# Kernel tuning notes

Measured on AMD Instinct MI355X. Metric: run time of the kernel, lower is better.

The kernel has to match this reference:

```python
import jax, jax.numpy as jnp
import numpy as np

N = 50000
E = 800000
F_IN = 128
HID = 64
G = 512
NEG_SLOPE = 0.2


def setup_inputs() -> dict:
    key = jax.random.key(0)
    ks = jax.random.split(key, 24)
    g = lambda i, shape: jax.random.normal(ks[i], shape, dtype=jnp.float32) * 0.1
    inp = {
        "x": jax.random.normal(ks[0], (N, F_IN), dtype=jnp.float32),
        "edge_index": jax.random.randint(ks[1], (2, E), 0, N),
        "edge_weight": jax.random.uniform(ks[2], (E, 1), dtype=jnp.float32),
        "batch": jnp.sort(jax.random.randint(ks[3], (N,), 0, G)),
        # layer 1
        "W1": g(4, (F_IN, HID)), "as1": g(5, (HID,)), "ad1": g(6, (HID,)),
        "We1": g(7, (1, HID)), "ae1": g(8, (HID,)), "b1": jnp.zeros((HID,), jnp.float32),
        # layer 2
        "W2": g(9, (HID, HID)), "as2": g(10, (HID,)), "ad2": g(11, (HID,)),
        "We2": g(12, (1, HID)), "ae2": g(13, (HID,)), "b2": jnp.zeros((HID,), jnp.float32),
        # layer 3
        "W3": g(14, (HID, HID)), "as3": g(15, (HID,)), "ad3": g(16, (HID,)),
        "We3": g(17, (1, HID)), "ae3": g(18, (HID,)), "b3": jnp.zeros((HID,), jnp.float32),
        # readout
        "lin_w": g(19, (HID, 1)), "lin_b": jnp.zeros((1,), jnp.float32),
    }
    return inp


def gat_layer(x, src, dst, eattr, W, att_s, att_d, We, att_e, bias):
    # x: [N,Fin]; src/dst: [Et]; eattr: [Et,1]
    h = x @ W                                  # [N,HID]
    a_src = h @ att_s                          # [N]
    a_dst = h @ att_d                          # [N]
    a_edge = (eattr @ We) @ att_e              # [Et]
    alpha = a_src[src] + a_dst[dst] + a_edge   # [Et]
    alpha = jax.nn.leaky_relu(alpha, NEG_SLOPE)
    # segment softmax over incoming edges of each dst node
    m = jax.ops.segment_max(alpha, dst, num_segments=N)
    alpha = jnp.exp(alpha - m[dst])
    s = jax.ops.segment_sum(alpha, dst, num_segments=N)
    alpha = alpha / (s[dst] + 1e-16)
    # weighted scatter-add of source features
    out = jax.ops.segment_sum(h[src] * alpha[:, None], dst, num_segments=N)
    return out + bias


def reference(x, edge_index, edge_weight, batch,
              W1, as1, ad1, We1, ae1, b1,
              W2, as2, ad2, We2, ae2, b2,
              W3, as3, ad3, We3, ae3, b3,
              lin_w, lin_b):
    # PyG GATConv default: add self-loops with edge_attr fill_value='mean'
    loop = jnp.arange(N)
    src = jnp.concatenate([edge_index[0], loop])
    dst = jnp.concatenate([edge_index[1], loop])
    mean_attr = jnp.mean(edge_weight, axis=0, keepdims=True)  # [1,1]
    eattr = jnp.concatenate([edge_weight, jnp.broadcast_to(mean_attr, (N, 1))], axis=0)

    h = gat_layer(x, src, dst, eattr, W1, as1, ad1, We1, ae1, b1)
    h = jax.nn.relu(h)
    h = gat_layer(h, src, dst, eattr, W2, as2, ad2, We2, ae2, b2)
    h = jax.nn.relu(h)
    h = gat_layer(h, src, dst, eattr, W3, as3, ad3, We3, ae3, b3)

    # global mean pool over graphs
    sums = jax.ops.segment_sum(h, batch, num_segments=G)          # [G,HID]
    counts = jax.ops.segment_sum(jnp.ones((N,), h.dtype), batch, num_segments=G)
    pooled = sums / jnp.maximum(counts, 1.0)[:, None]
    # dropout p=0.6 is identity at inference
    out = pooled @ lin_w + lin_b                                   # [G,1]
    return jax.nn.sigmoid(out)
```

## Files before the change

kernel.cpp:

```cpp
#include <hip/hip_runtime.h>
#include <math.h>

#define N_NODES 50000
#define N_EDGES 800000
#define F_IN_DIM 128
#define HID 64
#define NG 512
#define NEG 0.2f
#define SLICE ((N_NODES + 7) / 8)
#define EPB 2048
#define CAP 64

static __device__ __forceinline__ float wave_sum(float v) {
    for (int o = 32; o; o >>= 1) v += __shfl_xor(v, o, 64);
    return v;
}

static __device__ __forceinline__ unsigned short f2bf(float f) {
    union { float f; unsigned u; } v; v.f = f;
    unsigned r = (v.u + 0x7FFF + ((v.u >> 16) & 1)) >> 16;
    return (unsigned short)r;
}
static __device__ __forceinline__ float bf2f(unsigned short b) {
    union { unsigned u; float f; } v; v.u = ((unsigned)b) << 16;
    return v.f;
}

__global__ __launch_bounds__(256) void scatter_all_k(
        const int* __restrict__ ei, const float* __restrict__ ew,
        int* __restrict__ deg, unsigned* __restrict__ bucket,
        uint2* __restrict__ ovf, int* __restrict__ ovf_cnt,
        float* __restrict__ mean_acc,
        const float* __restrict__ We1, const float* __restrict__ ae1,
        const float* __restrict__ We2, const float* __restrict__ ae2,
        const float* __restrict__ We3, const float* __restrict__ ae3,
        float* __restrict__ ce) {
    int grp = blockIdx.x >> 3, slice = blockIdx.x & 7;
    int lo = slice * SLICE, hi = lo + SLICE;
    int base = grp * EPB;
    int lim = min(base + EPB, N_EDGES);
    float s = 0.f;
    for (int e = base + threadIdx.x; e < lim; e += 256) {
        int dst = ei[N_EDGES + e];
        if (slice == 0) s += ew[e];
        if (dst >= lo && dst < hi) {
            int src = ei[e];
            float w = ew[e];
            int pos = atomicAdd(&deg[dst], 1);
            unsigned entry = (unsigned)(src & 0xFFFF) | ((unsigned)f2bf(w) << 16);
            if (pos < CAP) bucket[(dst << 6) + pos] = entry;
            else { int op = atomicAdd(ovf_cnt, 1); ovf[op] = make_uint2((unsigned)dst, entry); }
        }
    }
    int lane = threadIdx.x & 63, wv = threadIdx.x >> 6;
    if (slice == 0) {
        s = wave_sum(s);
        __shared__ float tmp[4];
        if (lane == 0) tmp[wv] = s;
        __syncthreads();
        if (threadIdx.x == 0) atomicAdd(mean_acc, tmp[0] + tmp[1] + tmp[2] + tmp[3]);
    }
    if (blockIdx.x == 0 && wv >= 1) {
        const float* We = (wv == 1) ? We1 : (wv == 2) ? We2 : We3;
        const float* ae = (wv == 1) ? ae1 : (wv == 2) ? ae2 : ae3;
        float v = We[lane] * ae[lane];
        v = wave_sum(v);
        if (lane == 0) ce[wv - 1] = v;
    }
}

__global__ __launch_bounds__(256) void gemm_att_k(
        const float* __restrict__ X, int F,
        const float* __restrict__ W,
        const float* __restrict__ as_, const float* __restrict__ ad_,
        unsigned short* __restrict__ H, float* __restrict__ Asrc,
        float* __restrict__ Adst) {
    extern __shared__ float smem[];
    float* Ws = smem;
    float* Xs = smem + F * HID;
    const int tid = threadIdx.x;
    const int tx = tid & 15, ty = tid >> 4;
    const int rowBase = blockIdx.x * 64;

    {
        const float4* W4 = (const float4*)W;
        float4* Ws4 = (float4*)Ws;
        int n4 = (F * HID) >> 2;
        for (int i = tid; i < n4; i += 256) Ws4[i] = W4[i];
    }

    float4 acc0 = {0,0,0,0}, acc1 = {0,0,0,0}, acc2 = {0,0,0,0}, acc3 = {0,0,0,0};

    const int xrow = tid >> 2;
    const int xkq  = tid & 3;
    const int nkt = F >> 4;

    for (int kt = 0; kt < nkt; ++kt) {
        __syncthreads();
        int k0 = kt << 4;
        int grow = rowBase + xrow;
        float4 xv = {0,0,0,0};
        if (grow < N_NODES)
            xv = *(const float4*)(X + (size_t)grow * F + k0 + (xkq << 2));
        float* xd = Xs + xrow * 17 + (xkq << 2);
        xd[0] = xv.x; xd[1] = xv.y; xd[2] = xv.z; xd[3] = xv.w;
        __syncthreads();

        #pragma unroll
        for (int kk = 0; kk < 16; ++kk) {
            float4 b = *(const float4*)&Ws[(k0 + kk) * HID + (tx << 2)];
            float a0 = Xs[(ty * 4 + 0) * 17 + kk];
            float a1 = Xs[(ty * 4 + 1) * 17 + kk];
            float a2 = Xs[(ty * 4 + 2) * 17 + kk];
            float a3 = Xs[(ty * 4 + 3) * 17 + kk];
            acc0.x += a0 * b.x; acc0.y += a0 * b.y; acc0.z += a0 * b.z; acc0.w += a0 * b.w;
            acc1.x += a1 * b.x; acc1.y += a1 * b.y; acc1.z += a1 * b.z; acc1.w += a1 * b.w;
            acc2.x += a2 * b.x; acc2.y += a2 * b.y; acc2.z += a2 * b.z; acc2.w += a2 * b.w;
            acc3.x += a3 * b.x; acc3.y += a3 * b.y; acc3.z += a3 * b.z; acc3.w += a3 * b.w;
        }
    }

    float4 as4 = *(const float4*)(as_ + (tx << 2));
    float4 ad4 = *(const float4*)(ad_ + (tx << 2));
    float4 accs[4] = {acc0, acc1, acc2, acc3};
    #pragma unroll
    for (int i = 0; i < 4; ++i) {
        int row = rowBase + ty * 4 + i;
        if (row >= N_NODES) break;
        float4 a = accs[i];
        ushort4 hv;
        hv.x = f2bf(a.x); hv.y = f2bf(a.y); hv.z = f2bf(a.z); hv.w = f2bf(a.w);
        *(ushort4*)(H + (size_t)row * HID + (tx << 2)) = hv;
        float vs = a.x * as4.x + a.y * as4.y + a.z * as4.z + a.w * as4.w;
        float vd = a.x * ad4.x + a.y * ad4.y + a.z * ad4.z + a.w * ad4.w;
        #pragma unroll
        for (int o = 8; o; o >>= 1) { vs += __shfl_xor(vs, o, 64); vd += __shfl_xor(vd, o, 64); }
        if (tx == 0) { Asrc[row] = vs; Adst[row] = vd; }
    }
}

__global__ __launch_bounds__(256) void aggregate_k(
        const unsigned short* __restrict__ H, const int* __restrict__ degArr,
        const unsigned* __restrict__ bucket,
        const uint2* __restrict__ ovf, const int* __restrict__ ovf_cnt_p,
        const float* __restrict__ Asrc, const float* __restrict__ Adst,
        const float* __restrict__ ceArr, int ci,
        const float* __restrict__ mean_acc,
        const float* __restrict__ bias, float* __restrict__ Out,
        int do_relu) {
    __shared__ float lp[16][64];
    __shared__ int   ls[16][64];
    int wv = threadIdx.x >> 6, lane = threadIdx.x & 63;
    int qid = lane >> 4, qlane = lane & 15;
    int slot = wv * 4 + qid;
    int n = blockIdx.x * 16 + slot;
    if (n >= N_NODES) return;
    int deg = degArr[n];
    int start = n << 6;
    float c = ceArr[ci];
    float ad = Adst[n];
    float mv = mean_acc[0] * (1.0f / (float)N_EDGES);
    float4 acc = {0, 0, 0, 0};
    float denom;

    float a_self = Asrc[n] + ad + c * mv;
    a_self = (a_self > 0.f) ? a_self : NEG * a_self;
    float p_self = __expf(a_self);

    if (deg <= CAP) {
        float lsum = 0.f;
        #pragma unroll
        for (int t = 0; t < 4; ++t) {
            int j = qlane + (t << 4);
            float p = 0.f; int s = 0;
            if (j < deg) {
                unsigned e = bucket[start + j];
                s = e & 0xFFFF;
                float a = Asrc[s] + ad + c * bf2f((unsigned short)(e >> 16));
                a = (a > 0.f) ? a : NEG * a;
                p = __expf(a);
                lsum += p;
            }
            lp[slot][j] = p;
            ls[slot][j] = s;
        }
        if (qlane == 0) lsum += p_self;
        #pragma unroll
        for (int o = 1; o < 16; o <<= 1) lsum += __shfl_xor(lsum, o, 64);
        denom = lsum;
        __builtin_amdgcn_wave_barrier();
        int dpad = (deg + 7) & ~7;
        for (int j = 0; j < dpad; j += 8) {
            float4 p0 = *(float4*)&lp[slot][j];
            float4 p1 = *(float4*)&lp[slot][j + 4];
            int4 s0 = *(int4*)&ls[slot][j];
            int4 s1 = *(int4*)&ls[slot][j + 4];
            ushort4 r0 = *(const ushort4*)(H + (size_t)s0.x * HID + (qlane << 2));
            ushort4 r1 = *(const ushort4*)(H + (size_t)s0.y * HID + (qlane << 2));
            ushort4 r2 = *(const ushort4*)(H + (size_t)s0.z * HID + (qlane << 2));
            ushort4 r3 = *(const ushort4*)(H + (size_t)s0.w * HID + (qlane << 2));
            ushort4 r4 = *(const ushort4*)(H + (size_t)s1.x * HID + (qlane << 2));
            ushort4 r5 = *(const ushort4*)(H + (size_t)s1.y * HID + (qlane << 2));
            ushort4 r6 = *(const ushort4*)(H + (size_t)s1.z * HID + (qlane << 2));
            ushort4 r7 = *(const ushort4*)(H + (size_t)s1.w * HID + (qlane << 2));
            acc.x += p0.x*bf2f(r0.x) + p0.y*bf2f(r1.x) + p0.z*bf2f(r2.x) + p0.w*bf2f(r3.x)
                   + p1.x*bf2f(r4.x) + p1.y*bf2f(r5.x) + p1.z*bf2f(r6.x) + p1.w*bf2f(r7.x);
            acc.y += p0.x*bf2f(r0.y) + p0.y*bf2f(r1.y) + p0.z*bf2f(r2.y) + p0.w*bf2f(r3.y)
                   + p1.x*bf2f(r4.y) + p1.y*bf2f(r5.y) + p1.z*bf2f(r6.y) + p1.w*bf2f(r7.y);
            acc.z += p0.x*bf2f(r0.z) + p0.y*bf2f(r1.z) + p0.z*bf2f(r2.z) + p0.w*bf2f(r3.z)
                   + p1.x*bf2f(r4.z) + p1.y*bf2f(r5.z) + p1.z*bf2f(r6.z) + p1.w*bf2f(r7.z);
            acc.w += p0.x*bf2f(r0.w) + p0.y*bf2f(r1.w) + p0.z*bf2f(r2.w) + p0.w*bf2f(r3.w)
                   + p1.x*bf2f(r4.w) + p1.y*bf2f(r5.w) + p1.z*bf2f(r6.w) + p1.w*bf2f(r7.w);
        }
    } else {
        int novf = *ovf_cnt_p;
        float lsum = 0.f;
        #pragma unroll
        for (int t = 0; t < 4; ++t) {
            int j = qlane + (t << 4);
            unsigned e = bucket[start + j];
            int s = e & 0xFFFF;
            float a = Asrc[s] + ad + c * bf2f((unsigned short)(e >> 16));
            a = (a > 0.f) ? a : NEG * a;
            float p = __expf(a);
            lsum += p;
            lp[slot][j] = p;
            ls[slot][j] = s;
        }
        __builtin_amdgcn_wave_barrier();
        for (int j = 0; j < 64; j += 8) {
            float4 p0 = *(float4*)&lp[slot][j];
            float4 p1 = *(float4*)&lp[slot][j + 4];
            int4 s0 = *(int4*)&ls[slot][j];
            int4 s1 = *(int4*)&ls[slot][j + 4];
            ushort4 r0 = *(const ushort4*)(H + (size_t)s0.x * HID + (qlane << 2));
            ushort4 r1 = *(const ushort4*)(H + (size_t)s0.y * HID + (qlane << 2));
            ushort4 r2 = *(const ushort4*)(H + (size_t)s0.z * HID + (qlane << 2));
            ushort4 r3 = *(const ushort4*)(H + (size_t)s0.w * HID + (qlane << 2));
            ushort4 r4 = *(const ushort4*)(H + (size_t)s1.x * HID + (qlane << 2));
            ushort4 r5 = *(const ushort4*)(H + (size_t)s1.y * HID + (qlane << 2));
            ushort4 r6 = *(const ushort4*)(H + (size_t)s1.z * HID + (qlane << 2));
            ushort4 r7 = *(const ushort4*)(H + (size_t)s1.w * HID + (qlane << 2));
            acc.x += p0.x*bf2f(r0.x) + p0.y*bf2f(r1.x) + p0.z*bf2f(r2.x) + p0.w*bf2f(r3.x)
                   + p1.x*bf2f(r4.x) + p1.y*bf2f(r5.x) + p1.z*bf2f(r6.x) + p1.w*bf2f(r7.x);
            acc.y += p0.x*bf2f(r0.y) + p0.y*bf2f(r1.y) + p0.z*bf2f(r2.y) + p0.w*bf2f(r3.y)
                   + p1.x*bf2f(r4.y) + p1.y*bf2f(r5.y) + p1.z*bf2f(r6.y) + p1.w*bf2f(r7.y);
            acc.z += p0.x*bf2f(r0.z) + p0.y*bf2f(r1.z) + p0.z*bf2f(r2.z) + p0.w*bf2f(r3.z)
                   + p1.x*bf2f(r4.z) + p1.y*bf2f(r5.z) + p1.z*bf2f(r6.z) + p1.w*bf2f(r7.z);
            acc.w += p0.x*bf2f(r0.w) + p0.y*bf2f(r1.w) + p0.z*bf2f(r2.w) + p0.w*bf2f(r3.w)
                   + p1.x*bf2f(r4.w) + p1.y*bf2f(r5.w) + p1.z*bf2f(r6.w) + p1.w*bf2f(r7.w);
        }
        for (int i = 0; i < novf; ++i) {
            uint2 o = ovf[i];
            if ((int)o.x == n) {
                unsigned e = o.y;
                int s = e & 0xFFFF;
                float a = Asrc[s] + ad + c * bf2f((unsigned short)(e >> 16));
                a = (a > 0.f) ? a : NEG * a;
                float p = __expf(a);
                if (qlane == 0) lsum += p;
                ushort4 r = *(const ushort4*)(H + (size_t)s * HID + (qlane << 2));
                acc.x += p * bf2f(r.x); acc.y += p * bf2f(r.y);
                acc.z += p * bf2f(r.z); acc.w += p * bf2f(r.w);
            }
        }
        if (qlane == 0) lsum += p_self;
        #pragma unroll
        for (int o = 1; o < 16; o <<= 1) lsum += __shfl_xor(lsum, o, 64);
        denom = lsum;
    }

    {
        ushort4 r = *(const ushort4*)(H + (size_t)n * HID + (qlane << 2));
        acc.x += p_self * bf2f(r.x); acc.y += p_self * bf2f(r.y);
        acc.z += p_self * bf2f(r.z); acc.w += p_self * bf2f(r.w);
    }

    float inv = 1.f / (denom + 1e-16f);
    float4 b4 = *(const float4*)(bias + (qlane << 2));
    acc.x = acc.x * inv + b4.x;
    acc.y = acc.y * inv + b4.y;
    acc.z = acc.z * inv + b4.z;
    acc.w = acc.w * inv + b4.w;
    if (do_relu) {
        acc.x = fmaxf(acc.x, 0.f); acc.y = fmaxf(acc.y, 0.f);
        acc.z = fmaxf(acc.z, 0.f); acc.w = fmaxf(acc.w, 0.f);
    }
    *(float4*)(Out + (size_t)n * HID + (qlane << 2)) = acc;
}

__global__ __launch_bounds__(256) void pool_readout_k(
        const float* __restrict__ act, const int* __restrict__ batch,
        const float* __restrict__ lin_w, const float* __restrict__ lin_b,
        float* __restrict__ out) {
    int wv = threadIdx.x >> 6, lane = threadIdx.x & 63;
    int g = blockIdx.x * 4 + wv;
    if (g >= NG) return;
    int lo = 0, hi = N_NODES;
    while (lo < hi) { int m = (lo + hi) >> 1; if (batch[m] < g) lo = m + 1; else hi = m; }
    int start = lo;
    hi = N_NODES;
    while (lo < hi) { int m = (lo + hi) >> 1; if (batch[m] < g + 1) lo = m + 1; else hi = m; }
    int end = lo;
    float acc = 0.f;
    int n = start;
    for (; n + 4 <= end; n += 4) {
        float v0 = act[(size_t)n * HID + lane];
        float v1 = act[(size_t)(n + 1) * HID + lane];
        float v2 = act[(size_t)(n + 2) * HID + lane];
        float v3 = act[(size_t)(n + 3) * HID + lane];
        acc += v0 + v1 + v2 + v3;
    }
    for (; n < end; ++n) acc += act[(size_t)n * HID + lane];
    float cntf = (float)(end - start);
    float v = acc / fmaxf(cntf, 1.f) * lin_w[lane];
    v = wave_sum(v);
    if (lane == 0) {
        float z = v + lin_b[0];
        out[g] = 1.f / (1.f + __expf(-z));
    }
}

extern "C" void kernel_launch(void* const* d_in, const int* in_sizes, int n_in,
                              void* d_out, int out_size, void* d_ws, size_t ws_size,
                              hipStream_t stream) {
    const float* x     = (const float*)d_in[0];
    const int*   ei    = (const int*)d_in[1];
    const float* ew    = (const float*)d_in[2];
    const int*   batch = (const int*)d_in[3];
    const float* W1  = (const float*)d_in[4];
    const float* as1 = (const float*)d_in[5];
    const float* ad1 = (const float*)d_in[6];
    const float* We1 = (const float*)d_in[7];
    const float* ae1 = (const float*)d_in[8];
    const float* b1  = (const float*)d_in[9];
    const float* W2  = (const float*)d_in[10];
    const float* as2 = (const float*)d_in[11];
    const float* ad2 = (const float*)d_in[12];
    const float* We2 = (const float*)d_in[13];
    const float* ae2 = (const float*)d_in[14];
    const float* b2  = (const float*)d_in[15];
    const float* W3  = (const float*)d_in[16];
    const float* as3 = (const float*)d_in[17];
    const float* ad3 = (const float*)d_in[18];
    const float* We3 = (const float*)d_in[19];
    const float* ae3 = (const float*)d_in[20];
    const float* b3  = (const float*)d_in[21];
    const float* lin_w = (const float*)d_in[22];
    const float* lin_b = (const float*)d_in[23];
    float* out = (float*)d_out;

    char* w = (char*)d_ws;
    size_t off = 0;
    auto alloc = [&](size_t bytes) -> void* {
        void* p = w + off;
        off = (off + bytes + 255) & ~(size_t)255;
        return p;
    };
    int*   deg      = (int*)alloc(N_NODES * sizeof(int));
    float* mean_acc = (float*)alloc(sizeof(float));
    int*   ovf_cnt  = (int*)alloc(sizeof(int));
    size_t zero_bytes = off;
    float* ce      = (float*)alloc(4 * sizeof(float));
    unsigned* bucket = (unsigned*)alloc((size_t)N_NODES * CAP * sizeof(unsigned));
    uint2* ovf     = (uint2*)alloc((size_t)N_EDGES * sizeof(uint2));
    float* a_src   = (float*)alloc(N_NODES * sizeof(float));
    float* a_dst   = (float*)alloc(N_NODES * sizeof(float));
    unsigned short* hbuf = (unsigned short*)alloc((size_t)N_NODES * HID * sizeof(unsigned short));
    float* actA    = (float*)alloc((size_t)N_NODES * HID * sizeof(float));
    float* actB    = (float*)alloc((size_t)N_NODES * HID * sizeof(float));

    hipMemsetAsync(d_ws, 0, zero_bytes, stream);

    int xgrid = ((N_EDGES + EPB - 1) / EPB) * 8;
    scatter_all_k<<<xgrid, 256, 0, stream>>>(ei, ew, deg, bucket, ovf, ovf_cnt,
                                             mean_acc, We1, ae1, We2, ae2, We3, ae3, ce);

    int ggrid = (N_NODES + 63) / 64;
    int agrid = (N_NODES + 15) / 16;

    size_t lds1 = (size_t)(F_IN_DIM * HID + 64 * 17) * sizeof(float);
    size_t lds2 = (size_t)(HID * HID + 64 * 17) * sizeof(float);

    gemm_att_k<<<ggrid, 256, lds1, stream>>>(x, F_IN_DIM, W1, as1, ad1, hbuf, a_src, a_dst);
    aggregate_k<<<agrid, 256, 0, stream>>>(hbuf, deg, bucket, ovf, ovf_cnt,
                                           a_src, a_dst, ce, 0, mean_acc, b1, actA, 1);
    gemm_att_k<<<ggrid, 256, lds2, stream>>>(actA, HID, W2, as2, ad2, hbuf, a_src, a_dst);
    aggregate_k<<<agrid, 256, 0, stream>>>(hbuf, deg, bucket, ovf, ovf_cnt,
                                           a_src, a_dst, ce, 1, mean_acc, b2, actB, 1);
    gemm_att_k<<<ggrid, 256, lds2, stream>>>(actB, HID, W3, as3, ad3, hbuf, a_src, a_dst);
    aggregate_k<<<agrid, 256, 0, stream>>>(hbuf, deg, bucket, ovf, ovf_cnt,
                                           a_src, a_dst, ce, 2, mean_acc, b3, actA, 0);

    pool_readout_k<<<NG / 4, 256, 0, stream>>>(actA, batch, lin_w, lin_b, out);
}
```

Baseline: 286.1 us.

## Merge edge scatter and layer-1 GEMM into one heterogeneous launch

The edge-bucketing scatter kernel and the first-layer feature GEMM now share a single launch. Blocks below XGRID do the scatter and the remaining blocks compute the GEMM, since neither depends on the other. The layer-1 GEMM also changes from staging all of W in LDS to streaming 16-row K-tiles of W alongside X tiles, which cuts LDS use. The aim is to remove one launch and let the atomic-heavy scatter overlap with the compute-bound GEMM; the cost is an extra branch and mixed block behaviour within one grid.

```diff
diff --git a/kernel.cpp b/kernel.cpp
--- a/kernel.cpp
+++ b/kernel.cpp
@@ -10,6 +10,8 @@
 #define SLICE ((N_NODES + 7) / 8)
 #define EPB 2048
 #define CAP 64
+#define XGRID (((N_EDGES + EPB - 1) / EPB) * 8)
+#define GGRID ((N_NODES + 63) / 64)
 
 static __device__ __forceinline__ float wave_sum(float v) {
     for (int o = 32; o; o >>= 1) v += __shfl_xor(v, o, 64);
@@ -26,7 +28,7 @@
     return v.f;
 }
 
-__global__ __launch_bounds__(256) void scatter_all_k(
+__global__ __launch_bounds__(256) void scatter_gemm1_k(
         const int* __restrict__ ei, const float* __restrict__ ew,
         int* __restrict__ deg, unsigned* __restrict__ bucket,
         uint2* __restrict__ ovf, int* __restrict__ ovf_cnt,
@@ -34,38 +36,104 @@
         const float* __restrict__ We1, const float* __restrict__ ae1,
         const float* __restrict__ We2, const float* __restrict__ ae2,
         const float* __restrict__ We3, const float* __restrict__ ae3,
-        float* __restrict__ ce) {
-    int grp = blockIdx.x >> 3, slice = blockIdx.x & 7;
-    int lo = slice * SLICE, hi = lo + SLICE;
-    int base = grp * EPB;
-    int lim = min(base + EPB, N_EDGES);
-    float s = 0.f;
-    for (int e = base + threadIdx.x; e < lim; e += 256) {
-        int dst = ei[N_EDGES + e];
-        if (slice == 0) s += ew[e];
-        if (dst >= lo && dst < hi) {
-            int src = ei[e];
-            float w = ew[e];
-            int pos = atomicAdd(&deg[dst], 1);
-            unsigned entry = (unsigned)(src & 0xFFFF) | ((unsigned)f2bf(w) << 16);
-            if (pos < CAP) bucket[(dst << 6) + pos] = entry;
-            else { int op = atomicAdd(ovf_cnt, 1); ovf[op] = make_uint2((unsigned)dst, entry); }
-        }
-    }
-    int lane = threadIdx.x & 63, wv = threadIdx.x >> 6;
-    if (slice == 0) {
-        s = wave_sum(s);
-        __shared__ float tmp[4];
-        if (lane == 0) tmp[wv] = s;
+        float* __restrict__ ce,
+        const float* __restrict__ X, const float* __restrict__ W,
+        const float* __restrict__ as_, const float* __restrict__ ad_,
+        unsigned short* __restrict__ H, float* __restrict__ Asrc,
+        float* __restrict__ Adst) {
+    extern __shared__ float smem[];
+    const int tid = threadIdx.x;
+
+    if (blockIdx.x < XGRID) {
+        int grp = blockIdx.x >> 3, slice = blockIdx.x & 7;
+        int lo = slice * SLICE, hi = lo + SLICE;
+        int base = grp * EPB;
+        int lim = min(base + EPB, N_EDGES);
+        float s = 0.f;
+        for (int e = base + tid; e < lim; e += 256) {
+            int dst = ei[N_EDGES + e];
+            if (slice == 0) s += ew[e];
+            if (dst >= lo && dst < hi) {
+                int src = ei[e];
+                float w = ew[e];
+                int pos = atomicAdd(&deg[dst], 1);
+                unsigned entry = (unsigned)(src & 0xFFFF) | ((unsigned)f2bf(w) << 16);
+                if (pos < CAP) bucket[(dst << 6) + pos] = entry;
+                else { int op = atomicAdd(ovf_cnt, 1); ovf[op] = make_uint2((unsigned)dst, entry); }
+            }
+        }
+        int lane = tid & 63, wv = tid >> 6;
+        if (slice == 0) {
+            s = wave_sum(s);
+            if (lane == 0) smem[wv] = s;
+            __syncthreads();
+            if (tid == 0) atomicAdd(mean_acc, smem[0] + smem[1] + smem[2] + smem[3]);
+        }
+        if (blockIdx.x == 0 && wv >= 1) {
+            const float* We = (wv == 1) ? We1 : (wv == 2) ? We2 : We3;
+            const float* ae = (wv == 1) ? ae1 : (wv == 2) ? ae2 : ae3;
+            float v = We[lane] * ae[lane];
+            v = wave_sum(v);
+            if (lane == 0) ce[wv - 1] = v;
+        }
+        return;
+    }
+
+    float* Xs = smem;
+    float* Wt = smem + 64 * 17;
+    const int tx = tid & 15, ty = tid >> 4;
+    const int bid = blockIdx.x - XGRID;
+    const int rowBase = bid * 64;
+
+    float4 acc0 = {0,0,0,0}, acc1 = {0,0,0,0}, acc2 = {0,0,0,0}, acc3 = {0,0,0,0};
+    const int xrow = tid >> 2;
+    const int xkq  = tid & 3;
+    const float4* W4 = (const float4*)W;
+    float4* Wt4 = (float4*)Wt;
+
+    #pragma unroll 2
+    for (int kt = 0; kt < (F_IN_DIM >> 4); ++kt) {
         __syncthreads();
-        if (threadIdx.x == 0) atomicAdd(mean_acc, tmp[0] + tmp[1] + tmp[2] + tmp[3]);
-    }
-    if (blockIdx.x == 0 && wv >= 1) {
-        const float* We = (wv == 1) ? We1 : (wv == 2) ? We2 : We3;
-        const float* ae = (wv == 1) ? ae1 : (wv == 2) ? ae2 : ae3;
-        float v = We[lane] * ae[lane];
-        v = wave_sum(v);
-        if (lane == 0) ce[wv - 1] = v;
+        int k0 = kt << 4;
+        int grow = rowBase + xrow;
+        float4 xv = {0,0,0,0};
+        if (grow < N_NODES)
+            xv = *(const float4*)(X + (size_t)grow * F_IN_DIM + k0 + (xkq << 2));
+        float* xd = Xs + xrow * 17 + (xkq << 2);
+        xd[0] = xv.x; xd[1] = xv.y; xd[2] = xv.z; xd[3] = xv.w;
+        Wt4[tid] = W4[(kt << 8) + tid];
+        __syncthreads();
+
+        #pragma unroll
+        for (int kk = 0; kk < 16; ++kk) {
+            float4 b = *(const float4*)&Wt[kk * HID + (tx << 2)];
+            float a0 = Xs[(ty * 4 + 0) * 17 + kk];
+            float a1 = Xs[(ty * 4 + 1) * 17 + kk];
+            float a2 = Xs[(ty * 4 + 2) * 17 + kk];
+            float a3 = Xs[(ty * 4 + 3) * 17 + kk];
+            acc0.x += a0 * b.x; acc0.y += a0 * b.y; acc0.z += a0 * b.z; acc0.w += a0 * b.w;
+            acc1.x += a1 * b.x; acc1.y += a1 * b.y; acc1.z += a1 * b.z; acc1.w += a1 * b.w;
+            acc2.x += a2 * b.x; acc2.y += a2 * b.y; acc2.z += a2 * b.z; acc2.w += a2 * b.w;
+            acc3.x += a3 * b.x; acc3.y += a3 * b.y; acc3.z += a3 * b.z; acc3.w += a3 * b.w;
+        }
+    }
+
+    float4 as4 = *(const float4*)(as_ + (tx << 2));
+    float4 ad4 = *(const float4*)(ad_ + (tx << 2));
+    float4 accs[4] = {acc0, acc1, acc2, acc3};
+    #pragma unroll
+    for (int i = 0; i < 4; ++i) {
+        int row = rowBase + ty * 4 + i;
+        if (row >= N_NODES) break;
+        float4 a = accs[i];
+        ushort4 hv;
+        hv.x = f2bf(a.x); hv.y = f2bf(a.y); hv.z = f2bf(a.z); hv.w = f2bf(a.w);
+        *(ushort4*)(H + (size_t)row * HID + (tx << 2)) = hv;
+        float vs = a.x * as4.x + a.y * as4.y + a.z * as4.z + a.w * as4.w;
+        float vd = a.x * ad4.x + a.y * ad4.y + a.z * ad4.z + a.w * ad4.w;
+        #pragma unroll
+        for (int o = 8; o; o >>= 1) { vs += __shfl_xor(vs, o, 64); vd += __shfl_xor(vd, o, 64); }
+        if (tx == 0) { Asrc[row] = vs; Adst[row] = vd; }
     }
 }
 
@@ -372,23 +440,21 @@
 
     hipMemsetAsync(d_ws, 0, zero_bytes, stream);
 
-    int xgrid = ((N_EDGES + EPB - 1) / EPB) * 8;
-    scatter_all_k<<<xgrid, 256, 0, stream>>>(ei, ew, deg, bucket, ovf, ovf_cnt,
-                                             mean_acc, We1, ae1, We2, ae2, We3, ae3, ce);
-
-    int ggrid = (N_NODES + 63) / 64;
     int agrid = (N_NODES + 15) / 16;
-
-    size_t lds1 = (size_t)(F_IN_DIM * HID + 64 * 17) * sizeof(float);
-    size_t lds2 = (size_t)(HID * HID + 64 * 17) * sizeof(float);
-
-    gemm_att_k<<<ggrid, 256, lds1, stream>>>(x, F_IN_DIM, W1, as1, ad1, hbuf, a_src, a_dst);
+    size_t lds_f = (size_t)(64 * 17 + 16 * 64) * sizeof(float);
+    size_t lds2  = (size_t)(HID * HID + 64 * 17) * sizeof(float);
+
+    scatter_gemm1_k<<<XGRID + GGRID, 256, lds_f, stream>>>(
+        ei, ew, deg, bucket, ovf, ovf_cnt, mean_acc,
+        We1, ae1, We2, ae2, We3, ae3, ce,
+        x, W1, as1, ad1, hbuf, a_src, a_dst);
+
     aggregate_k<<<agrid, 256, 0, stream>>>(hbuf, deg, bucket, ovf, ovf_cnt,
                                            a_src, a_dst, ce, 0, mean_acc, b1, actA, 1);
-    gemm_att_k<<<ggrid, 256, lds2, stream>>>(actA, HID, W2, as2, ad2, hbuf, a_src, a_dst);
+    gemm_att_k<<<GGRID, 256, lds2, stream>>>(actA, HID, W2, as2, ad2, hbuf, a_src, a_dst);
     aggregate_k<<<agrid, 256, 0, stream>>>(hbuf, deg, bucket, ovf, ovf_cnt,
                                            a_src, a_dst, ce, 1, mean_acc, b2, actB, 1);
-    gemm_att_k<<<ggrid, 256, lds2, stream>>>(actB, HID, W3, as3, ad3, hbuf, a_src, a_dst);
+    gemm_att_k<<<GGRID, 256, lds2, stream>>>(actB, HID, W3, as3, ad3, hbuf, a_src, a_dst);
     aggregate_k<<<agrid, 256, 0, stream>>>(hbuf, deg, bucket, ovf, ovf_cnt,
                                            a_src, a_dst, ce, 2, mean_acc, b3, actA, 0);
 
```

Result: no change. 280.7 us (-1.9%).
